# Kernel optimization log

Hardware: AMD Instinct MI355X
Metric: run time of the kernel (lower is better)

Reference implementation:

```python
import jax, jax.numpy as jnp
import numpy as np

N_HEAD = 16
P_MIN, P_MAX = 1e-4, 1e3
V_MIN = 1e-10
SHIFT = 5.0


def setup_inputs() -> dict:
    key = jax.random.key(0)
    ks = jax.random.split(key, 4)
    B, T, C = 2, 2048, 1024
    x = jax.random.normal(ks[0], (B, T, C), dtype=jnp.float32)
    w_attn = jax.random.normal(ks[1], (C, 3 * C), dtype=jnp.float32) * 0.02
    b_attn = jnp.zeros((3 * C,), dtype=jnp.float32)
    w_proj = jax.random.normal(ks[2], (C, C), dtype=jnp.float32) * 0.02
    b_proj = jnp.zeros((C,), dtype=jnp.float32)
    p_param = jnp.ones((C,), dtype=jnp.float32)
    return {"x": x, "w_attn": w_attn, "b_attn": b_attn,
            "w_proj": w_proj, "b_proj": b_proj, "p_param": p_param}


def reference(x, w_attn, b_attn, w_proj, b_proj, p_param):
    B, T, C = x.shape
    H = N_HEAD
    d = C // H

    qkv = x @ w_attn + b_attn                      # [B,T,3C]
    q, k, v = jnp.split(qkv, 3, axis=2)

    # signed, clamped power exponent per channel: (sign(p)+0.5).sign() * clamp(|p|)
    p = jnp.sign(jnp.sign(p_param) + 0.5) * jnp.clip(jnp.abs(p_param), P_MIN, P_MAX)

    # log-power transform of V with max-subtraction over T for stability
    v = jnp.clip(jnp.abs(v + SHIFT), V_MIN, None)  # [B,T,C]
    z = p * jnp.log(v)
    z_max = jnp.max(z, axis=1, keepdims=True)      # [B,1,C]
    v = jnp.exp(z - z_max)

    # heads: [B,H,T,d]
    q = q.reshape(B, T, H, d).transpose(0, 2, 1, 3)
    k = k.reshape(B, T, H, d).transpose(0, 2, 1, 3)
    v = v.reshape(B, T, H, d).transpose(0, 2, 1, 3)

    scale = 1.0 / jnp.sqrt(jnp.float32(d))
    scores = jnp.einsum('bhqd,bhkd->bhqk', q, k) * scale
    causal = jnp.tril(jnp.ones((T, T), dtype=bool))
    scores = jnp.where(causal, scores, -jnp.inf)
    att = jax.nn.softmax(scores, axis=-1)
    mean = jnp.einsum('bhqk,bhkd->bhqd', att, v)   # [B,H,T,d]
    mean = mean.transpose(0, 2, 1, 3).reshape(B, T, C)

    # invert the log-power transform (generalized power mean)
    y = jnp.exp((z_max + jnp.log(mean)) / p) - SHIFT
    return y @ w_proj + b_proj
```

## Files before the change

kernel.cpp:

```cpp
#include <hip/hip_runtime.h>
#include <hip/hip_bf16.h>
#include <math.h>

constexpr int B_ = 2;
constexpr int T_ = 2048;
constexpr int C_ = 1024;
constexpr int H_ = 16;
constexpr int D_ = 64;
constexpr int M_ = B_ * T_;
constexpr float SHIFT_ = 5.0f;
constexpr float P_MIN_ = 1e-4f;
constexpr float P_MAX_ = 1e3f;
constexpr float V_MIN_ = 1e-10f;
constexpr float QS_ = 0.125f * 1.4426950408889634f;

typedef __attribute__((ext_vector_type(8))) short s16x8;
typedef __attribute__((ext_vector_type(8))) _Float16 h16x8;
typedef __attribute__((ext_vector_type(4))) float f32x4;
typedef unsigned short ushort_t;

__device__ __forceinline__ float clamp_p(float pp) {
    float s = (pp >= 0.f) ? 1.f : -1.f;
    return s * fminf(fmaxf(fabsf(pp), P_MIN_), P_MAX_);
}

__device__ __forceinline__ ushort_t f2h(float f) {
    _Float16 h = (_Float16)f;
    return __builtin_bit_cast(unsigned short, h);
}
__device__ __forceinline__ float h2f(ushort_t h) {
    return (float)__builtin_bit_cast(_Float16, h);
}

__device__ __forceinline__ float fast_exp2(float x) {
#if __has_builtin(__builtin_amdgcn_exp2f)
    return __builtin_amdgcn_exp2f(x);
#else
    return __expf(x * 0.6931471805599453f);
#endif
}

__device__ __forceinline__ void gload_lds16(const void* g, void* l) {
    __builtin_amdgcn_global_load_lds(
        (const __attribute__((address_space(1))) unsigned int*)g,
        (__attribute__((address_space(3))) unsigned int*)l, 16, 0, 0);
}

__device__ __forceinline__ void convT_body(const float* __restrict__ W,
                                           ushort_t* __restrict__ Wth,
                                           int N, int K, int bx, int by,
                                           int tid, float (*tile)[65]) {
    const int k0 = by * 64, n0 = bx * 64;
    const int tr = tid >> 4;
    const int tc4 = (tid & 15) * 4;
#pragma unroll
    for (int i = 0; i < 4; ++i) {
        float4 f = *(const float4*)&W[(size_t)(k0 + tr + i * 16) * N + n0 + tc4];
        tile[tr + i * 16][tc4 + 0] = f.x;
        tile[tr + i * 16][tc4 + 1] = f.y;
        tile[tr + i * 16][tc4 + 2] = f.z;
        tile[tr + i * 16][tc4 + 3] = f.w;
    }
    __syncthreads();
#pragma unroll
    for (int i = 0; i < 4; ++i) {
        int n = tr + i * 16;
        ushort4 h;
        h.x = f2h(tile[tc4 + 0][n]);
        h.y = f2h(tile[tc4 + 1][n]);
        h.z = f2h(tile[tc4 + 2][n]);
        h.w = f2h(tile[tc4 + 3][n]);
        *(ushort4*)&Wth[(size_t)(n0 + n) * K + k0 + tc4] = h;
    }
}

__global__ __launch_bounds__(256)
void prep_w(const float* __restrict__ x, const float* __restrict__ w_attn,
            const float* __restrict__ w_proj, ushort_t* __restrict__ xh,
            ushort_t* __restrict__ wth, ushort_t* __restrict__ wtp) {
    __shared__ float tile[64][65];
    const int blk = blockIdx.x;
    const int tid = threadIdx.x;
    if (blk < 4096) {
        int idx = blk * 256 + tid;
        float4 f = ((const float4*)x)[idx];
        ushort4 h;
        h.x = f2h(f.x); h.y = f2h(f.y); h.z = f2h(f.z); h.w = f2h(f.w);
        ((ushort4*)xh)[idx] = h;
    } else if (blk < 4096 + 768) {
        int sub = blk - 4096;
        convT_body(w_attn, wth, 3 * C_, C_, sub % 48, sub / 48, tid, tile);
    } else {
        int sub = blk - 4864;
        convT_body(w_proj, wtp, C_, C_, sub % 16, sub / 16, tid, tile);
    }
}

template <bool HALF_OUT>
__global__ __launch_bounds__(256)
void gemm1(const ushort_t* __restrict__ Ah, const ushort_t* __restrict__ Bh,
           const float* __restrict__ bias, void* __restrict__ Cout,
           int M, int N, int K, int qcols, float qscale) {
    __shared__ ushort_t Lds[2 * 2 * 128 * 32];

    const int tid = threadIdx.x;
    const int w = tid >> 6;
    const int lane = tid & 63;
    const int l16 = lane & 15;
    const int quad = lane >> 4;
    const int row0 = blockIdx.y * 128, col0 = blockIdx.x * 128;
    const int wr = w >> 1, wc = w & 1;

    const ushort_t* gb[8];
    ushort_t* lb[8];
#pragma unroll
    for (int j = 0; j < 8; ++j) {
        int q = j * 4 + w;
        int plane = q >> 4;
        int cc = q & 15;
        int sub = cc & 1;
        int r = (cc >> 1) * 16 + (lane >> 2);
        const ushort_t* src = plane ? Bh : Ah;
        int tb = plane ? col0 : row0;
        gb[j] = src + (size_t)(tb + r) * K + sub * 32 + (lane & 3) * 8;
        lb[j] = &Lds[plane * 8192 + sub * 4096 + r * 32 + (lane & 3) * 8];
    }

    f32x4 acc[4][4] = {};

    for (int k0 = 0; k0 < K; k0 += 64) {
        __syncthreads();
#pragma unroll
        for (int j = 0; j < 8; ++j)
            gload_lds16(gb[j] + k0, lb[j]);
        __syncthreads();

#pragma unroll
        for (int kk = 0; kk < 2; ++kk) {
            h16x8 af[4], bf[4];
#pragma unroll
            for (int mi = 0; mi < 4; ++mi)
                af[mi] = *(const h16x8*)&Lds[kk * 4096 + (wr * 64 + mi * 16 + l16) * 32 + quad * 8];
#pragma unroll
            for (int ni = 0; ni < 4; ++ni)
                bf[ni] = *(const h16x8*)&Lds[8192 + kk * 4096 + (wc * 64 + ni * 16 + l16) * 32 + quad * 8];
#pragma unroll
            for (int mi = 0; mi < 4; ++mi)
#pragma unroll
                for (int ni = 0; ni < 4; ++ni)
                    acc[mi][ni] = __builtin_amdgcn_mfma_f32_16x16x32_f16(bf[ni], af[mi], acc[mi][ni], 0, 0, 0);
        }
    }

    const float osc = (HALF_OUT && col0 < qcols) ? qscale : 1.0f;

#pragma unroll
    for (int mi = 0; mi < 4; ++mi) {
        int row = row0 + wr * 64 + mi * 16 + l16;
#pragma unroll
        for (int ni = 0; ni < 4; ++ni) {
            int colb = col0 + wc * 64 + ni * 16 + quad * 4;
            float4 bs = *(const float4*)&bias[colb];
            float v0 = acc[mi][ni][0] + bs.x;
            float v1 = acc[mi][ni][1] + bs.y;
            float v2 = acc[mi][ni][2] + bs.z;
            float v3 = acc[mi][ni][3] + bs.w;
            if (HALF_OUT) {
                ushort4 pk;
                pk.x = f2h(v0 * osc); pk.y = f2h(v1 * osc);
                pk.z = f2h(v2 * osc); pk.w = f2h(v3 * osc);
                *(ushort4*)&((ushort_t*)Cout)[(size_t)row * N + colb] = pk;
            } else {
                float4 pk = make_float4(v0, v1, v2, v3);
                *(float4*)&((float*)Cout)[(size_t)row * N + colb] = pk;
            }
        }
    }
}

__global__ __launch_bounds__(256)
void zmax_part(const ushort_t* __restrict__ qkvh, const float* __restrict__ p_param,
               float* __restrict__ zpart) {
    const int tch = blockIdx.x & 15;
    const int ctile = (blockIdx.x >> 4) & 15;
    const int b = blockIdx.x >> 8;
    const int col = threadIdx.x & 63;
    const int r = threadIdx.x >> 6;
    const int c = ctile * 64 + col;

    const float p = clamp_p(p_param[c]);
    const ushort_t* vp = qkvh + (size_t)b * T_ * 3 * C_
                       + (size_t)(tch * 128) * 3 * C_ + 2 * C_ + c;

    float lm = -INFINITY;
    for (int t = r; t < 128; t += 4) {
        float v = h2f(vp[(size_t)t * 3 * C_]);
        float z = p * __logf(fmaxf(fabsf(v + SHIFT_), V_MIN_));
        lm = fmaxf(lm, z);
    }
    __shared__ float red[4][64];
    red[r][col] = lm;
    __syncthreads();
    if (threadIdx.x < 64) {
        float m = fmaxf(fmaxf(red[0][threadIdx.x], red[1][threadIdx.x]),
                        fmaxf(red[2][threadIdx.x], red[3][threadIdx.x]));
        zpart[((size_t)b * 16 + tch) * C_ + ctile * 64 + threadIdx.x] = m;
    }
}

__global__ __launch_bounds__(256)
void prep_kv(const ushort_t* __restrict__ qkvh, const float* __restrict__ p_param,
             const float* __restrict__ zpart, float* __restrict__ zmax,
             ushort_t* __restrict__ kbf, ushort_t* __restrict__ vtbf) {
    __shared__ ushort_t VtL[64 * 72];
    __shared__ float zm_l[64];

    const int blk = blockIdx.x;
    const int tt = blk & 31;
    const int bh = blk >> 5;
    const int b = bh >> 4;
    const int h = bh & 15;
    const int t0 = tt * 64;

    const int tl = threadIdx.x >> 2;
    const int c0 = (threadIdx.x & 3) * 16;
    const int g0 = c0 >> 3;
    const int ptl = ((tl >> 5) & 1) * 32 + ((tl >> 2) & 3) * 8
                  + ((tl >> 4) & 1) * 4 + (tl & 3);

    if (threadIdx.x < 64) {
        int c = h * D_ + threadIdx.x;
        float m = -INFINITY;
#pragma unroll
        for (int ch = 0; ch < 16; ++ch)
            m = fmaxf(m, zpart[((size_t)b * 16 + ch) * C_ + c]);
        zm_l[threadIdx.x] = m;
        zmax[b * C_ + c] = m;
    }
    __syncthreads();

    const size_t rowbase = (size_t)(b * T_ + t0 + tl) * 3 * C_ + h * D_;

    {
        const ushort_t* ksrc = qkvh + rowbase + C_ + c0;
        s16x8 k0v = *(const s16x8*)&ksrc[0];
        s16x8 k1v = *(const s16x8*)&ksrc[8];
        size_t krow = ((size_t)bh * T_ + t0 + tl) * 64;
        *(s16x8*)&kbf[krow + ((g0)     ^ (tl & 7)) * 8] = k0v;
        *(s16x8*)&kbf[krow + ((g0 + 1) ^ (tl & 7)) * 8] = k1v;
    }

    {
        const ushort_t* vsrc = qkvh + rowbase + 2 * C_ + c0;
        ushort_t tv[16];
        *(s16x8*)&tv[0] = *(const s16x8*)&vsrc[0];
        *(s16x8*)&tv[8] = *(const s16x8*)&vsrc[8];
#pragma unroll
        for (int q = 0; q < 16; ++q) {
            int j = c0 + q;
            float p = clamp_p(p_param[h * D_ + j]);
            float v = h2f(tv[q]);
            float z = p * __logf(fmaxf(fabsf(v + SHIFT_), V_MIN_));
            float val = __expf(z - zm_l[j]);
            VtL[j * 72 + ptl] = f2h(val);
        }
    }
    __syncthreads();
    {
        const int d = tl;
        s16x8 r0 = *(const s16x8*)&VtL[d * 72 + c0];
        s16x8 r1 = *(const s16x8*)&VtL[d * 72 + c0 + 8];
        size_t vbase = ((size_t)bh * 32 + tt) * 4096 + (size_t)d * 64;
        *(s16x8*)&vtbf[vbase + ((g0)     ^ (d & 7)) * 8] = r0;
        *(s16x8*)&vtbf[vbase + ((g0 + 1) ^ (d & 7)) * 8] = r1;
    }
}

__device__ __forceinline__ void load_frag(h16x8 kf[2][4], const ushort_t* tile,
                                          int l16, int sg0, int sg1) {
#pragma unroll
    for (int nt = 0; nt < 4; ++nt) {
        kf[0][nt] = *(const h16x8*)&tile[(nt * 16 + l16) * 64 + sg0];
        kf[1][nt] = *(const h16x8*)&tile[(nt * 16 + l16) * 64 + sg1];
    }
}

__device__ __forceinline__ void tile_body2(const h16x8 qf[2][2], const h16x8 kf[2][4],
        const h16x8 vf[2][4], const h16x8 ones, bool diag, int l16, int quad, int qh,
        f32x4 O[2][4], f32x4 Ol[2]) {
#pragma unroll
    for (int m = 0; m < 2; ++m) {
        f32x4 s[4] = {};
#pragma unroll
        for (int nt = 0; nt < 4; ++nt) {
            s[nt] = __builtin_amdgcn_mfma_f32_16x16x32_f16(kf[0][nt], qf[m][0], s[nt], 0, 0, 0);
            s[nt] = __builtin_amdgcn_mfma_f32_16x16x32_f16(kf[1][nt], qf[m][1], s[nt], 0, 0, 0);
        }

        if (diag) {
            int row = qh * 32 + m * 16 + l16;
#pragma unroll
            for (int nt = 0; nt < 4; ++nt)
#pragma unroll
                for (int r = 0; r < 4; ++r) {
                    int col = nt * 16 + quad * 4 + r;
                    if (col > row) s[nt][r] = -3.0e38f;
                }
        }

#pragma unroll
        for (int ks = 0; ks < 2; ++ks) {
            ushort_t t8[8];
#pragma unroll
            for (int r = 0; r < 4; ++r) {
                t8[r]     = f2h(fast_exp2(s[2 * ks][r]));
                t8[4 + r] = f2h(fast_exp2(s[2 * ks + 1][r]));
            }
            h16x8 pa = *(const h16x8*)t8;
            Ol[m] = __builtin_amdgcn_mfma_f32_16x16x32_f16(ones, pa, Ol[m], 0, 0, 0);
#pragma unroll
            for (int nt = 0; nt < 4; ++nt)
                O[m][nt] = __builtin_amdgcn_mfma_f32_16x16x32_f16(vf[ks][nt], pa, O[m][nt], 0, 0, 0);
        }
    }
}

__global__ __launch_bounds__(256, 2)
void attn_mfma(const ushort_t* __restrict__ qkvh,
               const ushort_t* __restrict__ kbf, const ushort_t* __restrict__ vtbf,
               const float* __restrict__ zmax, const float* __restrict__ p_param,
               ushort_t* __restrict__ yh) {
    __shared__ float Osum[2][64][33];
    __shared__ float Lsum[2][32];
    __shared__ float zm_l[64], ip_l[64];
    __shared__ ushort_t Ytile[64][72];

    const int tid = threadIdx.x;
    const int w = tid >> 6;
    const int lane = tid & 63;
    const int l16 = lane & 15;
    const int quad = lane >> 4;
    const int qh = w >> 1;
    const int kp = w & 1;

    const int qt = 31 - (blockIdx.x >> 5);
    const int bh = blockIdx.x & 31;
    const int b = bh >> 4;
    const int h = bh & 15;
    const int q0 = qt * 64;

    if (tid < 64) {
        int c = h * D_ + tid;
        zm_l[tid] = zmax[b * C_ + c];
        ip_l[tid] = 1.f / clamp_p(p_param[c]);
    }

    const int sg0 = ((0 + quad) ^ (l16 & 7)) * 8;
    const int sg1 = ((4 + quad) ^ (l16 & 7)) * 8;

    f32x4 O[2][4] = {};
    f32x4 Ol[2] = {};

    h16x8 ones;
#pragma unroll
    for (int i = 0; i < 8; ++i) ones[i] = (_Float16)1.0f;

    h16x8 qf[2][2];
#pragma unroll
    for (int m = 0; m < 2; ++m) {
        const int qrow = q0 + qh * 32 + m * 16 + l16;
        const ushort_t* qrp = qkvh + (size_t)(b * T_ + qrow) * 3 * C_ + h * D_;
#pragma unroll
        for (int ks = 0; ks < 2; ++ks)
            qf[m][ks] = *(const h16x8*)&qrp[ks * 32 + quad * 8];
    }

    const ushort_t* khead = kbf + (size_t)bh * T_ * 64;
    const ushort_t* vhead = vtbf + (size_t)bh * 32 * 4096;

    if (kp <= qt) {
        h16x8 kfA[2][4], kfB[2][4], vf[2][4];
        load_frag(kfA, khead + (size_t)kp * 4096, l16, sg0, sg1);

        for (int kt = kp; kt <= qt; kt += 4) {
            load_frag(vf, vhead + (size_t)kt * 4096, l16, sg0, sg1);
            int ktB = (kt + 2 <= qt) ? kt + 2 : kt;
            load_frag(kfB, khead + (size_t)ktB * 4096, l16, sg0, sg1);
            tile_body2(qf, kfA, vf, ones, kt == qt, l16, quad, qh, O, Ol);
            if (kt + 2 > qt) break;
            load_frag(vf, vhead + (size_t)(kt + 2) * 4096, l16, sg0, sg1);
            int ktA = (kt + 4 <= qt) ? kt + 4 : kt + 2;
            load_frag(kfA, khead + (size_t)ktA * 4096, l16, sg0, sg1);
            tile_body2(qf, kfB, vf, ones, kt + 2 == qt, l16, quad, qh, O, Ol);
        }
    }

    if (kp == 0) {
#pragma unroll
        for (int m = 0; m < 2; ++m) {
#pragma unroll
            for (int nt = 0; nt < 4; ++nt)
#pragma unroll
                for (int r = 0; r < 4; ++r)
                    Osum[qh][nt * 16 + quad * 4 + r][m * 16 + l16] = O[m][nt][r];
            if (quad == 0) Lsum[qh][m * 16 + l16] = Ol[m][0];
        }
    }
    __syncthreads();
    if (kp == 1) {
#pragma unroll
        for (int m = 0; m < 2; ++m) {
            int ql = m * 16 + l16;
            float inv_den = 1.f / (Ol[m][0] + Lsum[qh][ql]);
#pragma unroll
            for (int nt = 0; nt < 4; ++nt) {
                ushort4 pk;
#pragma unroll
                for (int r = 0; r < 4; ++r) {
                    int d = nt * 16 + quad * 4 + r;
                    float mean = (O[m][nt][r] + Osum[qh][d][ql]) * inv_den;
                    float y = __expf((zm_l[d] + __logf(mean)) * ip_l[d]) - SHIFT_;
                    ((ushort_t*)&pk)[r] = f2h(y);
                }
                *(ushort4*)&Ytile[qh * 32 + ql][nt * 16 + quad * 4] = pk;
            }
        }
    }
    __syncthreads();

#pragma unroll
    for (int it = 0; it < 2; ++it) {
        int c = it * 256 + tid;
        int row = c >> 3;
        int part = c & 7;
        s16x8 v = *(const s16x8*)&Ytile[row][part * 8];
        *(s16x8*)&yh[(size_t)(b * T_ + q0 + row) * C_ + h * D_ + part * 8] = v;
    }
}

extern "C" void kernel_launch(void* const* d_in, const int* in_sizes, int n_in,
                              void* d_out, int out_size, void* d_ws, size_t ws_size,
                              hipStream_t stream) {
    const float* x      = (const float*)d_in[0];
    const float* w_attn = (const float*)d_in[1];
    const float* b_attn = (const float*)d_in[2];
    const float* w_proj = (const float*)d_in[3];
    const float* b_proj = (const float*)d_in[4];
    const float* p_par  = (const float*)d_in[5];
    float* out = (float*)d_out;

    char* ws = (char*)d_ws;
    ushort_t* qkvh = (ushort_t*)ws;
    ushort_t* xh   = qkvh + (size_t)M_ * 3 * C_;
    ushort_t* wth  = xh + (size_t)M_ * C_;
    ushort_t* wtp  = wth + (size_t)3 * C_ * C_;
    float* zmax = (float*)(wtp + (size_t)C_ * C_);
    ushort_t* kbf  = (ushort_t*)(zmax + B_ * C_);
    ushort_t* vtbf = kbf + (size_t)B_ * H_ * T_ * 64;
    float* zpart = (float*)(vtbf + (size_t)B_ * H_ * T_ * 64);

    prep_w<<<4096 + 768 + 256, 256, 0, stream>>>(x, w_attn, w_proj, xh, wth, wtp);
    gemm1<true><<<dim3(3 * C_ / 128, M_ / 128), 256, 0, stream>>>(
        xh, wth, b_attn, qkvh, M_, 3 * C_, C_, C_, QS_);
    zmax_part<<<B_ * 16 * 16, 256, 0, stream>>>(qkvh, p_par, zpart);
    prep_kv<<<B_ * H_ * 32, 256, 0, stream>>>(qkvh, p_par, zpart, zmax, kbf, vtbf);
    attn_mfma<<<B_ * H_ * (T_ / 64), 256, 0, stream>>>(qkvh, kbf, vtbf,
                                                       zmax, p_par, xh);
    gemm1<false><<<dim3(C_ / 128, M_ / 128), 256, 0, stream>>>(
        xh, wtp, b_proj, out, M_, C_, C_, 0, 1.0f);
}
```

Baseline: 202.5 us.

## Fuse K relayout and V column max/min reduction into QKV GEMM epilogue

The QKV GEMM epilogue now writes K straight into the swizzled per-head layout and reduces per-column max/min of |v+shift| with atomics. This removes the zmax_part kernel and the K copy in prep_kv. The V stats become the log-space max through monotonicity of log and the sign of p, and one extra block in prep_w initialises the atomic buffers. It trades two kernel launches and a re-read of the V and K planes for atomic traffic and a heavier epilogue in the GEMM.

```diff
diff --git a/kernel.cpp b/kernel.cpp
--- a/kernel.cpp
+++ b/kernel.cpp
@@ -77,7 +77,8 @@
 __global__ __launch_bounds__(256)
 void prep_w(const float* __restrict__ x, const float* __restrict__ w_attn,
             const float* __restrict__ w_proj, ushort_t* __restrict__ xh,
-            ushort_t* __restrict__ wth, ushort_t* __restrict__ wtp) {
+            ushort_t* __restrict__ wth, ushort_t* __restrict__ wtp,
+            unsigned* __restrict__ umax, unsigned* __restrict__ umin) {
     __shared__ float tile[64][65];
     const int blk = blockIdx.x;
     const int tid = threadIdx.x;
@@ -90,17 +91,24 @@
     } else if (blk < 4096 + 768) {
         int sub = blk - 4096;
         convT_body(w_attn, wth, 3 * C_, C_, sub % 48, sub / 48, tid, tile);
-    } else {
+    } else if (blk < 4096 + 768 + 256) {
         int sub = blk - 4864;
         convT_body(w_proj, wtp, C_, C_, sub % 16, sub / 16, tid, tile);
-    }
-}
-
-template <bool HALF_OUT>
+    } else {
+#pragma unroll
+        for (int j = 0; j < 8; ++j) {
+            umax[j * 256 + tid] = 0u;
+            umin[j * 256 + tid] = 0xFFFFFFFFu;
+        }
+    }
+}
+
+template <int MODE>
 __global__ __launch_bounds__(256)
 void gemm1(const ushort_t* __restrict__ Ah, const ushort_t* __restrict__ Bh,
            const float* __restrict__ bias, void* __restrict__ Cout,
-           int M, int N, int K, int qcols, float qscale) {
+           ushort_t* __restrict__ kbf, unsigned* __restrict__ umax,
+           unsigned* __restrict__ umin, int M, int N, int K, float qscale) {
     __shared__ ushort_t Lds[2 * 2 * 128 * 32];
 
     const int tid = threadIdx.x;
@@ -152,66 +160,108 @@
         }
     }
 
-    const float osc = (HALF_OUT && col0 < qcols) ? qscale : 1.0f;
-
-#pragma unroll
-    for (int mi = 0; mi < 4; ++mi) {
-        int row = row0 + wr * 64 + mi * 16 + l16;
-#pragma unroll
-        for (int ni = 0; ni < 4; ++ni) {
-            int colb = col0 + wc * 64 + ni * 16 + quad * 4;
-            float4 bs = *(const float4*)&bias[colb];
-            float v0 = acc[mi][ni][0] + bs.x;
-            float v1 = acc[mi][ni][1] + bs.y;
-            float v2 = acc[mi][ni][2] + bs.z;
-            float v3 = acc[mi][ni][3] + bs.w;
-            if (HALF_OUT) {
-                ushort4 pk;
-                pk.x = f2h(v0 * osc); pk.y = f2h(v1 * osc);
-                pk.z = f2h(v2 * osc); pk.w = f2h(v3 * osc);
-                *(ushort4*)&((ushort_t*)Cout)[(size_t)row * N + colb] = pk;
-            } else {
-                float4 pk = make_float4(v0, v1, v2, v3);
+    if (MODE == 0) {
+#pragma unroll
+        for (int mi = 0; mi < 4; ++mi) {
+            int row = row0 + wr * 64 + mi * 16 + l16;
+#pragma unroll
+            for (int ni = 0; ni < 4; ++ni) {
+                int colb = col0 + wc * 64 + ni * 16 + quad * 4;
+                float4 bs = *(const float4*)&bias[colb];
+                float4 pk = make_float4(acc[mi][ni][0] + bs.x, acc[mi][ni][1] + bs.y,
+                                        acc[mi][ni][2] + bs.z, acc[mi][ni][3] + bs.w);
                 *(float4*)&((float*)Cout)[(size_t)row * N + colb] = pk;
             }
         }
+    } else {
+        const int plane = col0 >> 10;
+        if (plane == 1) {
+            const int b = row0 >> 11;
+#pragma unroll
+            for (int mi = 0; mi < 4; ++mi) {
+                int row = row0 + wr * 64 + mi * 16 + l16;
+                int t = row & (T_ - 1);
+#pragma unroll
+                for (int ni = 0; ni < 4; ++ni) {
+                    int cp = (col0 - C_) + wc * 64 + ni * 16 + quad * 4;
+                    float4 bs = *(const float4*)&bias[C_ + cp];
+                    ushort4 pk;
+                    pk.x = f2h(acc[mi][ni][0] + bs.x);
+                    pk.y = f2h(acc[mi][ni][1] + bs.y);
+                    pk.z = f2h(acc[mi][ni][2] + bs.z);
+                    pk.w = f2h(acc[mi][ni][3] + bs.w);
+                    int hh = cp >> 6, d = cp & 63;
+                    int g = d >> 3, off = d & 7;
+                    size_t addr = ((size_t)((b << 4) + hh) * T_ + t) * 64
+                                + ((g ^ (t & 7)) << 3) + off;
+                    *(ushort4*)&kbf[addr] = pk;
+                }
+            }
+        } else {
+            const float osc = (plane == 0) ? qscale : 1.0f;
+            float cmx[4][4], cmn[4][4];
+            if (plane == 2) {
+#pragma unroll
+                for (int ni = 0; ni < 4; ++ni)
+#pragma unroll
+                    for (int r = 0; r < 4; ++r) { cmx[ni][r] = 0.f; cmn[ni][r] = 3.4e38f; }
+            }
+#pragma unroll
+            for (int mi = 0; mi < 4; ++mi) {
+                int row = row0 + wr * 64 + mi * 16 + l16;
+#pragma unroll
+                for (int ni = 0; ni < 4; ++ni) {
+                    int colb = col0 + wc * 64 + ni * 16 + quad * 4;
+                    float4 bs = *(const float4*)&bias[colb];
+                    float v0 = acc[mi][ni][0] + bs.x;
+                    float v1 = acc[mi][ni][1] + bs.y;
+                    float v2 = acc[mi][ni][2] + bs.z;
+                    float v3 = acc[mi][ni][3] + bs.w;
+                    if (plane == 2) {
+                        float a0 = fabsf(v0 + SHIFT_), a1 = fabsf(v1 + SHIFT_);
+                        float a2 = fabsf(v2 + SHIFT_), a3 = fabsf(v3 + SHIFT_);
+                        cmx[ni][0] = fmaxf(cmx[ni][0], a0); cmn[ni][0] = fminf(cmn[ni][0], a0);
+                        cmx[ni][1] = fmaxf(cmx[ni][1], a1); cmn[ni][1] = fminf(cmn[ni][1], a1);
+                        cmx[ni][2] = fmaxf(cmx[ni][2], a2); cmn[ni][2] = fminf(cmn[ni][2], a2);
+                        cmx[ni][3] = fmaxf(cmx[ni][3], a3); cmn[ni][3] = fminf(cmn[ni][3], a3);
+                    }
+                    ushort4 pk;
+                    pk.x = f2h(v0 * osc); pk.y = f2h(v1 * osc);
+                    pk.z = f2h(v2 * osc); pk.w = f2h(v3 * osc);
+                    *(ushort4*)&((ushort_t*)Cout)[(size_t)row * N + colb] = pk;
+                }
+            }
+            if (plane == 2) {
+#pragma unroll
+                for (int ni = 0; ni < 4; ++ni)
+#pragma unroll
+                    for (int r = 0; r < 4; ++r) {
+#pragma unroll
+                        for (int s = 1; s < 16; s <<= 1) {
+                            cmx[ni][r] = fmaxf(cmx[ni][r], __shfl_xor(cmx[ni][r], s));
+                            cmn[ni][r] = fminf(cmn[ni][r], __shfl_xor(cmn[ni][r], s));
+                        }
+                    }
+                if (l16 == 0) {
+                    const int b = row0 >> 11;
+#pragma unroll
+                    for (int ni = 0; ni < 4; ++ni)
+#pragma unroll
+                        for (int r = 0; r < 4; ++r) {
+                            int cv = (col0 - 2 * C_) + wc * 64 + ni * 16 + quad * 4 + r;
+                            atomicMax(&umax[b * C_ + cv], __float_as_uint(cmx[ni][r]));
+                            atomicMin(&umin[b * C_ + cv], __float_as_uint(cmn[ni][r]));
+                        }
+                }
+            }
+        }
     }
 }
 
 __global__ __launch_bounds__(256)
-void zmax_part(const ushort_t* __restrict__ qkvh, const float* __restrict__ p_param,
-               float* __restrict__ zpart) {
-    const int tch = blockIdx.x & 15;
-    const int ctile = (blockIdx.x >> 4) & 15;
-    const int b = blockIdx.x >> 8;
-    const int col = threadIdx.x & 63;
-    const int r = threadIdx.x >> 6;
-    const int c = ctile * 64 + col;
-
-    const float p = clamp_p(p_param[c]);
-    const ushort_t* vp = qkvh + (size_t)b * T_ * 3 * C_
-                       + (size_t)(tch * 128) * 3 * C_ + 2 * C_ + c;
-
-    float lm = -INFINITY;
-    for (int t = r; t < 128; t += 4) {
-        float v = h2f(vp[(size_t)t * 3 * C_]);
-        float z = p * __logf(fmaxf(fabsf(v + SHIFT_), V_MIN_));
-        lm = fmaxf(lm, z);
-    }
-    __shared__ float red[4][64];
-    red[r][col] = lm;
-    __syncthreads();
-    if (threadIdx.x < 64) {
-        float m = fmaxf(fmaxf(red[0][threadIdx.x], red[1][threadIdx.x]),
-                        fmaxf(red[2][threadIdx.x], red[3][threadIdx.x]));
-        zpart[((size_t)b * 16 + tch) * C_ + ctile * 64 + threadIdx.x] = m;
-    }
-}
-
-__global__ __launch_bounds__(256)
-void prep_kv(const ushort_t* __restrict__ qkvh, const float* __restrict__ p_param,
-             const float* __restrict__ zpart, float* __restrict__ zmax,
-             ushort_t* __restrict__ kbf, ushort_t* __restrict__ vtbf) {
+void prep_v(const ushort_t* __restrict__ qkvh, const float* __restrict__ p_param,
+            const unsigned* __restrict__ umax, const unsigned* __restrict__ umin,
+            float* __restrict__ zmax, ushort_t* __restrict__ vtbf) {
     __shared__ ushort_t VtL[64 * 72];
     __shared__ float zm_l[64];
 
@@ -230,28 +280,18 @@
 
     if (threadIdx.x < 64) {
         int c = h * D_ + threadIdx.x;
-        float m = -INFINITY;
-#pragma unroll
-        for (int ch = 0; ch < 16; ++ch)
-            m = fmaxf(m, zpart[((size_t)b * 16 + ch) * C_ + c]);
-        zm_l[threadIdx.x] = m;
-        zmax[b * C_ + c] = m;
+        float pm = clamp_p(p_param[c]);
+        float mp = fmaxf(__uint_as_float(umax[b * C_ + c]), V_MIN_);
+        float mn = fmaxf(__uint_as_float(umin[b * C_ + c]), V_MIN_);
+        float zm = (pm >= 0.f) ? pm * __logf(mp) : pm * __logf(mn);
+        zm_l[threadIdx.x] = zm;
+        zmax[b * C_ + c] = zm;
     }
     __syncthreads();
 
-    const size_t rowbase = (size_t)(b * T_ + t0 + tl) * 3 * C_ + h * D_;
-
     {
-        const ushort_t* ksrc = qkvh + rowbase + C_ + c0;
-        s16x8 k0v = *(const s16x8*)&ksrc[0];
-        s16x8 k1v = *(const s16x8*)&ksrc[8];
-        size_t krow = ((size_t)bh * T_ + t0 + tl) * 64;
-        *(s16x8*)&kbf[krow + ((g0)     ^ (tl & 7)) * 8] = k0v;
-        *(s16x8*)&kbf[krow + ((g0 + 1) ^ (tl & 7)) * 8] = k1v;
-    }
-
-    {
-        const ushort_t* vsrc = qkvh + rowbase + 2 * C_ + c0;
+        const ushort_t* vsrc = qkvh + (size_t)(b * T_ + t0 + tl) * 3 * C_
+                             + 2 * C_ + h * D_ + c0;
         ushort_t tv[16];
         *(s16x8*)&tv[0] = *(const s16x8*)&vsrc[0];
         *(s16x8*)&tv[8] = *(const s16x8*)&vsrc[8];
@@ -457,15 +497,16 @@
     float* zmax = (float*)(wtp + (size_t)C_ * C_);
     ushort_t* kbf  = (ushort_t*)(zmax + B_ * C_);
     ushort_t* vtbf = kbf + (size_t)B_ * H_ * T_ * 64;
-    float* zpart = (float*)(vtbf + (size_t)B_ * H_ * T_ * 64);
-
-    prep_w<<<4096 + 768 + 256, 256, 0, stream>>>(x, w_attn, w_proj, xh, wth, wtp);
-    gemm1<true><<<dim3(3 * C_ / 128, M_ / 128), 256, 0, stream>>>(
-        xh, wth, b_attn, qkvh, M_, 3 * C_, C_, C_, QS_);
-    zmax_part<<<B_ * 16 * 16, 256, 0, stream>>>(qkvh, p_par, zpart);
-    prep_kv<<<B_ * H_ * 32, 256, 0, stream>>>(qkvh, p_par, zpart, zmax, kbf, vtbf);
+    unsigned* umax = (unsigned*)(vtbf + (size_t)B_ * H_ * T_ * 64);
+    unsigned* umin = umax + B_ * C_;
+
+    prep_w<<<4096 + 768 + 256 + 1, 256, 0, stream>>>(x, w_attn, w_proj,
+                                                     xh, wth, wtp, umax, umin);
+    gemm1<1><<<dim3(3 * C_ / 128, M_ / 128), 256, 0, stream>>>(
+        xh, wth, b_attn, qkvh, kbf, umax, umin, M_, 3 * C_, C_, QS_);
+    prep_v<<<B_ * H_ * 32, 256, 0, stream>>>(qkvh, p_par, umax, umin, zmax, vtbf);
     attn_mfma<<<B_ * H_ * (T_ / 64), 256, 0, stream>>>(qkvh, kbf, vtbf,
                                                        zmax, p_par, xh);
-    gemm1<false><<<dim3(C_ / 128, M_ / 128), 256, 0, stream>>>(
-        xh, wtp, b_proj, out, M_, C_, C_, 0, 1.0f);
-}
+    gemm1<0><<<dim3(C_ / 128, M_ / 128), 256, 0, stream>>>(
+        xh, wtp, b_proj, out, nullptr, nullptr, nullptr, M_, C_, C_, 1.0f);
+}
```

New measurement: 199.7 us. Within noise of the previous version (-1.4%).
